# Performance work log

Measured on AMD Instinct MI355X. Metric: run time of the kernel, lower is better.

The kernel has to match this reference:

```python
import jax, jax.numpy as jnp
import numpy as np

B, S, F, H = 8, 4096, 1024, 1024


def setup_inputs() -> dict:
    key = jax.random.key(0)
    ks = jax.random.split(key, 7)
    sc = 1.0 / np.sqrt(F)
    return {
        "x": jax.random.normal(ks[0], (B, S, F), dtype=jnp.float32),
        "Wq": jax.random.normal(ks[1], (F, F), dtype=jnp.float32) * sc,
        "bq": jax.random.normal(ks[2], (F,), dtype=jnp.float32) * sc,
        "Wk": jax.random.normal(ks[3], (F, F), dtype=jnp.float32) * sc,
        "bk": jax.random.normal(ks[4], (F,), dtype=jnp.float32) * sc,
        "Wv": jax.random.normal(ks[5], (H, F), dtype=jnp.float32) * sc,
        "bv": jax.random.normal(ks[6], (H,), dtype=jnp.float32) * sc,
    }


def reference(x, Wq, bq, Wk, bk, Wv, bv):
    # q, k: [B, S, F]  (torch Linear: x @ W.T + b, W stored [out, in])
    q = jnp.einsum("bsf,of->bso", x, Wq) + bq
    k = jnp.einsum("bsf,of->bso", x, Wk) + bk
    # attention over the feature axis: logits [B, F, F], no scaling
    logits = jnp.einsum("bsf,bsg->bfg", q, k)
    weights = jax.nn.softmax(logits, axis=-1)
    # attn_out = x @ weights : [B, S, F]
    attn_out = jnp.einsum("bsf,bfg->bsg", x, weights)
    # value projection F -> H
    out = jnp.einsum("bsf,hf->bsh", attn_out, Wv) + bv
    return out
```

## Files before the change

kernel.cpp:

```cpp
#include <hip/hip_runtime.h>
#include <hip/hip_bf16.h>

#define DEVI __device__ __forceinline__

typedef _Float16 f16_t;
typedef f16_t f16x8 __attribute__((ext_vector_type(8)));
typedef f16_t f16x4 __attribute__((ext_vector_type(4)));
typedef float f32x4 __attribute__((ext_vector_type(4)));

static constexpr int B_ = 8, S_ = 4096, F_ = 1024, H_ = 1024;

DEVI void gload_lds16(const void* g, void* l) {
  __builtin_amdgcn_global_load_lds(
      (const __attribute__((address_space(1))) unsigned int*)g,
      (__attribute__((address_space(3))) unsigned int*)l, 16, 0, 0);
}

template <int MODE>
__global__ __launch_bounds__(256, 2) void gemm_nt(
    const f16_t* __restrict__ A0, const f16_t* __restrict__ A1,
    const f16_t* __restrict__ A2, const f16_t* __restrict__ B0,
    const f16_t* __restrict__ B1, const f16_t* __restrict__ B2,
    void* __restrict__ Cout, const float* __restrict__ bias,
    int Kseg, int nseg, int ldA, int ldB,
    long sA, long sB, long sC, int ldc, long noff)
{
  const int bz = blockIdx.z;
  const f16_t* Ab[3] = {A0 + (size_t)bz * sA, A1 + (size_t)bz * sA,
                        A2 + (size_t)bz * sA};
  const f16_t* Bb[3] = {B0 + (size_t)bz * sB, B1 + (size_t)bz * sB,
                        B2 + (size_t)bz * sB};
  const int tid = threadIdx.x;
  const int wave = tid >> 6, lane = tid & 63;
  const int wr = wave >> 1, wc = wave & 1;
  const long bm = (long)blockIdx.x * 128, bn = (long)blockIdx.y * 128;

  __shared__ f16_t As[128 * 64];
  __shared__ f16_t Bs[128 * 64];

  f32x4 acc[4][4] = {};

  const int l16 = lane * 16;
  const size_t lda_b = (size_t)ldA * 2;
  const size_t ldb_b = (size_t)ldB * 2;

  for (int seg = 0; seg < nseg; ++seg) {
    const char* Aseg = (const char*)Ab[seg];
    const char* Bseg = (const char*)Bb[seg];
    for (int kt = 0; kt < Kseg; kt += 64) {
      __syncthreads();
#pragma unroll
      for (int j = 0; j < 4; ++j) {
        const int base = j * 4096 + wave * 1024;
        const int off = base + l16;
        const int row = off >> 7, colb = off & 127;
        gload_lds16(Aseg + (size_t)(bm + row) * lda_b + (size_t)kt * 2 + colb,
                    (char*)As + base);
      }
#pragma unroll
      for (int j = 0; j < 4; ++j) {
        const int base = j * 4096 + wave * 1024;
        const int off = base + l16;
        const int row = off >> 7, colb = off & 127;
        gload_lds16(Bseg + (size_t)(bn + row) * ldb_b + (size_t)kt * 2 + colb,
                    (char*)Bs + base);
      }
      __syncthreads();
#pragma unroll
      for (int kk = 0; kk < 2; ++kk) {
        f16x8 af[4], bg[4];
#pragma unroll
        for (int m = 0; m < 4; ++m) {
          const int row = wr * 64 + m * 16 + (lane & 15);
          af[m] = *(const f16x8*)((const char*)As + row * 128 + kk * 64 + (lane >> 4) * 16);
        }
#pragma unroll
        for (int n = 0; n < 4; ++n) {
          const int row = wc * 64 + n * 16 + (lane & 15);
          bg[n] = *(const f16x8*)((const char*)Bs + row * 128 + kk * 64 + (lane >> 4) * 16);
        }
#pragma unroll
        for (int m = 0; m < 4; ++m)
#pragma unroll
          for (int n = 0; n < 4; ++n)
            acc[m][n] = __builtin_amdgcn_mfma_f32_16x16x32_f16(af[m], bg[n], acc[m][n], 0, 0, 0);
      }
    }
  }

  const int r0 = (lane >> 4) * 4;
  const int c0 = lane & 15;
#pragma unroll
  for (int m = 0; m < 4; ++m) {
#pragma unroll
    for (int n = 0; n < 4; ++n) {
      const long col = bn + wc * 64 + n * 16 + c0;
      float bcol = 0.f;
      if (MODE == 3) bcol = bias[col];
#pragma unroll
      for (int j = 0; j < 4; ++j) {
        const long row = bm + wr * 64 + m * 16 + r0 + j;
        const float vv = acc[m][n][j];
        if (MODE == 0 || MODE == 3) {
          ((float*)Cout)[(long)bz * sC + row * ldc + col] = vv + bcol;
        } else if (MODE == 1) {
          ((f16_t*)Cout)[(long)bz * sC + row * ldc + col] = (f16_t)vv;
        } else {
          f16_t hi = (f16_t)vv;
          float lo = vv - (float)hi;
          f16_t* C = (f16_t*)Cout + (long)bz * sC + row * ldc + col;
          C[0] = hi;
          C[noff] = (f16_t)lo;
        }
      }
    }
  }
}

__global__ __launch_bounds__(256) void conv_x(const float* __restrict__ x,
                                              f16_t* __restrict__ Xf,
                                              f16_t* __restrict__ Xt)
{
  const int b = blockIdx.z;
  const int s0 = blockIdx.x * 64, f0 = blockIdx.y * 64;
  const float* xb = x + (size_t)b * S_ * F_;
  f16_t* Xfb = Xf + (size_t)b * S_ * F_;
  f16_t* Xtb = Xt + (size_t)b * S_ * F_;
  __shared__ f16_t tile[64][72];
  const int tid = threadIdx.x;
#pragma unroll
  for (int i = 0; i < 4; ++i) {
    const int idx = i * 256 + tid;
    const int r = idx >> 4, c4 = idx & 15;
    f32x4 v = *(const f32x4*)(xb + (size_t)(s0 + r) * F_ + f0 + c4 * 4);
    f16x4 h;
    h[0] = (f16_t)v[0]; h[1] = (f16_t)v[1];
    h[2] = (f16_t)v[2]; h[3] = (f16_t)v[3];
    *(f16x4*)(Xfb + (size_t)(s0 + r) * F_ + f0 + c4 * 4) = h;
    *(f16x4*)(&tile[r][c4 * 4]) = h;
  }
  __syncthreads();
#pragma unroll
  for (int i = 0; i < 2; ++i) {
    const int idx = i * 256 + tid;
    const int r = idx >> 3, c8 = idx & 7;
    f16x8 o;
#pragma unroll
    for (int j = 0; j < 8; ++j) o[j] = tile[c8 * 8 + j][r];
    *(f16x8*)(Xtb + (size_t)(f0 + r) * S_ + s0 + c8 * 8) = o;
  }
}

__global__ __launch_bounds__(256) void conv_w(const float* __restrict__ Wq,
    const float* __restrict__ Wk, const float* __restrict__ Wv,
    f16_t* __restrict__ Wqh, f16_t* __restrict__ Wql,
    f16_t* __restrict__ Wkh, f16_t* __restrict__ Wkl,
    f16_t* __restrict__ Wvh)
{
  const int idx = blockIdx.x * 256 + threadIdx.x;
  const int e = idx * 4;
  f32x4 q = *(const f32x4*)(Wq + e);
  f32x4 k = *(const f32x4*)(Wk + e);
  f32x4 w = *(const f32x4*)(Wv + e);
  f16x4 qh, ql, kh, kl, wh;
#pragma unroll
  for (int j = 0; j < 4; ++j) {
    f16_t h = (f16_t)q[j];
    qh[j] = h; ql[j] = (f16_t)(q[j] - (float)h);
    h = (f16_t)k[j];
    kh[j] = h; kl[j] = (f16_t)(k[j] - (float)h);
    wh[j] = (f16_t)w[j];
  }
  *(f16x4*)(Wqh + e) = qh;
  *(f16x4*)(Wql + e) = ql;
  *(f16x4*)(Wkh + e) = kh;
  *(f16x4*)(Wkl + e) = kl;
  *(f16x4*)(Wvh + e) = wh;
}

__global__ __launch_bounds__(256) void colsum_k(const f16_t* __restrict__ Xt,
                                                float* __restrict__ c)
{
  const int gw = blockIdx.x * 4 + (threadIdx.x >> 6);
  const int lane = threadIdx.x & 63;
  const f16_t* row = Xt + (size_t)gw * S_;
  float s = 0.f;
#pragma unroll
  for (int rep = 0; rep < 8; ++rep) {
    f16x8 v = *(const f16x8*)(row + rep * 512 + lane * 8);
#pragma unroll
    for (int j = 0; j < 8; ++j) s += (float)v[j];
  }
#pragma unroll
  for (int off = 32; off > 0; off >>= 1) s += __shfl_down(s, off);
  if (lane == 0) c[gw] = s;
}

__global__ __launch_bounds__(256) void uv_k(const float* __restrict__ Wq,
    const float* __restrict__ Wk, const float* __restrict__ c,
    float* __restrict__ u, float* __restrict__ v)
{
  const int gw = blockIdx.x * 4 + (threadIdx.x >> 6);
  const int lane = threadIdx.x & 63;
  const int sel = gw >> 13;
  const int id = gw & 8191;
  const int b = id >> 10, f = id & 1023;
  const float* W = sel ? Wk : Wq;
  const float* wrow = W + (size_t)f * 1024;
  const float* crow = c + b * 1024;
  float s = 0.f;
#pragma unroll
  for (int rep = 0; rep < 4; ++rep) {
    f32x4 wv = *(const f32x4*)(wrow + rep * 256 + lane * 4);
    f32x4 cv = *(const f32x4*)(crow + rep * 256 + lane * 4);
    s += wv[0] * cv[0] + wv[1] * cv[1] + wv[2] * cv[2] + wv[3] * cv[3];
  }
#pragma unroll
  for (int off = 32; off > 0; off >>= 1) s += __shfl_down(s, off);
  if (lane == 0) { (sel ? v : u)[id] = s; }
}

__global__ __launch_bounds__(256) void softmax_k(const float* __restrict__ L,
    const float* __restrict__ bq, const float* __restrict__ bk,
    const float* __restrict__ u, const float* __restrict__ v,
    f16_t* __restrict__ W)
{
  const int row = blockIdx.x;
  const int b = row >> 10, f = row & 1023;
  const float* Lr = L + (size_t)row * 1024;
  const float uq = u[row], bqf = bq[f];
  const int tid = threadIdx.x;
  const int wave = tid >> 6, lane = tid & 63;

  f32x4 lv  = *(const f32x4*)(Lr + tid * 4);
  f32x4 bkv = *(const f32x4*)(bk + tid * 4);
  f32x4 vv  = *(const f32x4*)(v + b * 1024 + tid * 4);
  float lg[4];
#pragma unroll
  for (int j = 0; j < 4; ++j)
    lg[j] = lv[j] + uq * bkv[j] + bqf * (vv[j] + 4096.f * bkv[j]);

  __shared__ float red[8];
  float m = fmaxf(fmaxf(lg[0], lg[1]), fmaxf(lg[2], lg[3]));
#pragma unroll
  for (int off = 32; off > 0; off >>= 1) m = fmaxf(m, __shfl_down(m, off));
  if (lane == 0) red[wave] = m;
  __syncthreads();
  m = fmaxf(fmaxf(red[0], red[1]), fmaxf(red[2], red[3]));

  float p[4], s = 0.f;
#pragma unroll
  for (int j = 0; j < 4; ++j) { p[j] = __expf(lg[j] - m); s += p[j]; }
#pragma unroll
  for (int off = 32; off > 0; off >>= 1) s += __shfl_down(s, off);
  if (lane == 0) red[4 + wave] = s;
  __syncthreads();
  s = red[4] + red[5] + red[6] + red[7];
  const float inv = 1.f / s;
  f16x4 o;
#pragma unroll
  for (int j = 0; j < 4; ++j) o[j] = (f16_t)(p[j] * inv);
  *(f16x4*)(W + (size_t)row * 1024 + tid * 4) = o;
}

extern "C" void kernel_launch(void* const* d_in, const int* in_sizes, int n_in,
                              void* d_out, int out_size, void* d_ws, size_t ws_size,
                              hipStream_t stream)
{
  const float* x  = (const float*)d_in[0];
  const float* Wq = (const float*)d_in[1];
  const float* bq = (const float*)d_in[2];
  const float* Wk = (const float*)d_in[3];
  const float* bk = (const float*)d_in[4];
  const float* Wv = (const float*)d_in[5];
  const float* bv = (const float*)d_in[6];
  float* out = (float*)d_out;

  const size_t MB = 1024ull * 1024ull;
  char* ws = (char*)d_ws;
  f16_t* Xf  = (f16_t*)(ws);
  f16_t* Xt  = (f16_t*)(ws + 64 * MB);
  float* Lf  = (float*)(ws + 64 * MB);
  f16_t* Th  = (f16_t*)(ws + 96 * MB);
  f16_t* Tl  = (f16_t*)(ws + 112 * MB);
  f16_t* Wqh = (f16_t*)(ws + 128 * MB);
  f16_t* Wql = (f16_t*)(ws + 130 * MB);
  f16_t* Wkh = (f16_t*)(ws + 132 * MB);
  f16_t* Wkl = (f16_t*)(ws + 134 * MB);
  f16_t* Wvh = (f16_t*)(ws + 136 * MB);
  float* csum = (float*)(ws + 138 * MB);
  float* uvec = (float*)(ws + 138 * MB + 64 * 1024);
  float* vvec = (float*)(ws + 138 * MB + 128 * 1024);
  f16_t* Gh  = (f16_t*)(ws + 139 * MB);
  f16_t* Gl  = (f16_t*)(ws + 155 * MB);
  f16_t* Wsm = (f16_t*)(ws + 139 * MB);
  f16_t* Mt  = (f16_t*)(ws + 155 * MB);

  if (ws_size < 171 * MB) return;

  const long M1 = 1024L * 1024L;
  const long noffG = 8L * M1;
  const long noffT = 8L * M1;

  dim3 blk(256);
  conv_x<<<dim3(64, 16, 8), blk, 0, stream>>>(x, Xf, Xt);
  conv_w<<<dim3(1024), blk, 0, stream>>>(Wq, Wk, Wv, Wqh, Wql, Wkh, Wkl, Wvh);
  colsum_k<<<dim3(2048), blk, 0, stream>>>(Xt, csum);
  uv_k<<<dim3(4096), blk, 0, stream>>>(Wq, Wk, csum, uvec, vvec);
  gemm_nt<2><<<dim3(8, 8, 8), blk, 0, stream>>>(Xt, Xt, Xt, Xt, Xt, Xt,
      Gh, nullptr, 4096, 1, 4096, 4096,
      (long)F_ * S_, (long)F_ * S_, M1, 1024, noffG);
  gemm_nt<2><<<dim3(8, 8, 8), blk, 0, stream>>>(Wqh, Wql, Wqh, Gh, Gh, Gl,
      Th, nullptr, 1024, 3, 1024, 1024,
      0L, M1, M1, 1024, noffT);
  gemm_nt<0><<<dim3(8, 8, 8), blk, 0, stream>>>(Th, Tl, Th, Wkh, Wkh, Wkl,
      Lf, nullptr, 1024, 3, 1024, 1024,
      M1, 0L, M1, 1024, 0L);
  softmax_k<<<dim3(8192), blk, 0, stream>>>(Lf, bq, bk, uvec, vvec, Wsm);
  gemm_nt<1><<<dim3(8, 8, 8), blk, 0, stream>>>(Wvh, Wvh, Wvh, Wsm, Wsm, Wsm,
      Mt, nullptr, 1024, 1, 1024, 1024,
      0L, M1, M1, 1024, 0L);
  gemm_nt<3><<<dim3(32, 8, 8), blk, 0, stream>>>(Xf, Xf, Xf, Mt, Mt, Mt,
      out, bv, 1024, 1, 1024, 1024,
      (long)S_ * F_, M1, (long)S_ * H_, 1024, 0L);
}
```

Measured before the change: 641.3 us.

## Double-buffer LDS tiles and use 8-wave blocks in the GEMM kernel

The shared GEMM kernel now double-buffers its A and B LDS tiles and issues the next K-step's global-to-LDS loads before computing the current step. This aims to overlap memory latency with MFMA work and replaces two barriers per step with one. Blocks grow to 512 threads (8 waves in a 2x4 layout), so each wave owns a 64x32 sub-tile. The risks are doubled LDS use, which caps resident blocks, and tighter register limits from the new launch bounds, which could cause spills.

```diff
diff --git a/kernel.cpp b/kernel.cpp
--- a/kernel.cpp
+++ b/kernel.cpp
@@ -17,7 +17,7 @@
 }
 
 template <int MODE>
-__global__ __launch_bounds__(256, 2) void gemm_nt(
+__global__ __launch_bounds__(512, 4) void gemm_nt(
     const f16_t* __restrict__ A0, const f16_t* __restrict__ A1,
     const f16_t* __restrict__ A2, const f16_t* __restrict__ B0,
     const f16_t* __restrict__ B1, const f16_t* __restrict__ B2,
@@ -26,66 +26,72 @@
     long sA, long sB, long sC, int ldc, long noff)
 {
   const int bz = blockIdx.z;
-  const f16_t* Ab[3] = {A0 + (size_t)bz * sA, A1 + (size_t)bz * sA,
-                        A2 + (size_t)bz * sA};
-  const f16_t* Bb[3] = {B0 + (size_t)bz * sB, B1 + (size_t)bz * sB,
-                        B2 + (size_t)bz * sB};
   const int tid = threadIdx.x;
   const int wave = tid >> 6, lane = tid & 63;
-  const int wr = wave >> 1, wc = wave & 1;
+  const int wr = wave >> 2, wc = wave & 3;
   const long bm = (long)blockIdx.x * 128, bn = (long)blockIdx.y * 128;
 
-  __shared__ f16_t As[128 * 64];
-  __shared__ f16_t Bs[128 * 64];
-
-  f32x4 acc[4][4] = {};
-
-  const int l16 = lane * 16;
+  __shared__ f16_t As[2][128 * 64];
+  __shared__ f16_t Bs[2][128 * 64];
+
+  f32x4 acc[4][2] = {};
+
   const size_t lda_b = (size_t)ldA * 2;
   const size_t ldb_b = (size_t)ldB * 2;
 
-  for (int seg = 0; seg < nseg; ++seg) {
-    const char* Aseg = (const char*)Ab[seg];
-    const char* Bseg = (const char*)Bb[seg];
-    for (int kt = 0; kt < Kseg; kt += 64) {
-      __syncthreads();
-#pragma unroll
-      for (int j = 0; j < 4; ++j) {
-        const int base = j * 4096 + wave * 1024;
-        const int off = base + l16;
-        const int row = off >> 7, colb = off & 127;
-        gload_lds16(Aseg + (size_t)(bm + row) * lda_b + (size_t)kt * 2 + colb,
-                    (char*)As + base);
+  const char* A0b = (const char*)(A0 + (size_t)bz * sA);
+  const char* A1b = (const char*)(A1 + (size_t)bz * sA);
+  const char* A2b = (const char*)(A2 + (size_t)bz * sA);
+  const char* B0b = (const char*)(B0 + (size_t)bz * sB);
+  const char* B1b = (const char*)(B1 + (size_t)bz * sB);
+  const char* B2b = (const char*)(B2 + (size_t)bz * sB);
+
+  const int nsteps = nseg * (Kseg >> 6);
+
+  auto stage = [&](int buf, int sg, int kt) {
+    const char* Ap = (sg == 0) ? A0b : (sg == 1) ? A1b : A2b;
+    const char* Bp = (sg == 0) ? B0b : (sg == 1) ? B1b : B2b;
+    Ap += (size_t)kt * 2;
+    Bp += (size_t)kt * 2;
+#pragma unroll
+    for (int j = 0; j < 2; ++j) {
+      const int base = wave * 2048 + j * 1024;
+      const int off = base + lane * 16;
+      const int row = off >> 7, colb = off & 127;
+      gload_lds16(Ap + (size_t)(bm + row) * lda_b + colb, (char*)As[buf] + base);
+      gload_lds16(Bp + (size_t)(bn + row) * ldb_b + colb, (char*)Bs[buf] + base);
+    }
+  };
+
+  stage(0, 0, 0);
+  __syncthreads();
+
+  int seg = 0, kt = 0, cur = 0;
+  for (int t = 0; t < nsteps; ++t) {
+    int kt2 = kt + 64, seg2 = seg;
+    if (kt2 == Kseg) { kt2 = 0; seg2 = seg + 1; }
+    if (t + 1 < nsteps) stage(cur ^ 1, seg2, kt2);
+#pragma unroll
+    for (int kk = 0; kk < 2; ++kk) {
+      f16x8 af[4], bg[2];
+#pragma unroll
+      for (int m = 0; m < 4; ++m) {
+        const int row = wr * 64 + m * 16 + (lane & 15);
+        af[m] = *(const f16x8*)((const char*)As[cur] + row * 128 + kk * 64 + (lane >> 4) * 16);
       }
 #pragma unroll
-      for (int j = 0; j < 4; ++j) {
-        const int base = j * 4096 + wave * 1024;
-        const int off = base + l16;
-        const int row = off >> 7, colb = off & 127;
-        gload_lds16(Bseg + (size_t)(bn + row) * ldb_b + (size_t)kt * 2 + colb,
-                    (char*)Bs + base);
+      for (int n = 0; n < 2; ++n) {
+        const int row = wc * 32 + n * 16 + (lane & 15);
+        bg[n] = *(const f16x8*)((const char*)Bs[cur] + row * 128 + kk * 64 + (lane >> 4) * 16);
       }
-      __syncthreads();
-#pragma unroll
-      for (int kk = 0; kk < 2; ++kk) {
-        f16x8 af[4], bg[4];
-#pragma unroll
-        for (int m = 0; m < 4; ++m) {
-          const int row = wr * 64 + m * 16 + (lane & 15);
-          af[m] = *(const f16x8*)((const char*)As + row * 128 + kk * 64 + (lane >> 4) * 16);
-        }
-#pragma unroll
-        for (int n = 0; n < 4; ++n) {
-          const int row = wc * 64 + n * 16 + (lane & 15);
-          bg[n] = *(const f16x8*)((const char*)Bs + row * 128 + kk * 64 + (lane >> 4) * 16);
-        }
-#pragma unroll
-        for (int m = 0; m < 4; ++m)
-#pragma unroll
-          for (int n = 0; n < 4; ++n)
-            acc[m][n] = __builtin_amdgcn_mfma_f32_16x16x32_f16(af[m], bg[n], acc[m][n], 0, 0, 0);
-      }
+#pragma unroll
+      for (int m = 0; m < 4; ++m)
+#pragma unroll
+        for (int n = 0; n < 2; ++n)
+          acc[m][n] = __builtin_amdgcn_mfma_f32_16x16x32_f16(af[m], bg[n], acc[m][n], 0, 0, 0);
     }
+    __syncthreads();
+    cur ^= 1; seg = seg2; kt = kt2;
   }
 
   const int r0 = (lane >> 4) * 4;
@@ -93,8 +99,8 @@
 #pragma unroll
   for (int m = 0; m < 4; ++m) {
 #pragma unroll
-    for (int n = 0; n < 4; ++n) {
-      const long col = bn + wc * 64 + n * 16 + c0;
+    for (int n = 0; n < 2; ++n) {
+      const long col = bn + wc * 32 + n * 16 + c0;
       float bcol = 0.f;
       if (MODE == 3) bcol = bias[col];
 #pragma unroll
@@ -303,24 +309,25 @@
   const long noffT = 8L * M1;
 
   dim3 blk(256);
+  dim3 gblk(512);
   conv_x<<<dim3(64, 16, 8), blk, 0, stream>>>(x, Xf, Xt);
   conv_w<<<dim3(1024), blk, 0, stream>>>(Wq, Wk, Wv, Wqh, Wql, Wkh, Wkl, Wvh);
   colsum_k<<<dim3(2048), blk, 0, stream>>>(Xt, csum);
   uv_k<<<dim3(4096), blk, 0, stream>>>(Wq, Wk, csum, uvec, vvec);
-  gemm_nt<2><<<dim3(8, 8, 8), blk, 0, stream>>>(Xt, Xt, Xt, Xt, Xt, Xt,
+  gemm_nt<2><<<dim3(8, 8, 8), gblk, 0, stream>>>(Xt, Xt, Xt, Xt, Xt, Xt,
       Gh, nullptr, 4096, 1, 4096, 4096,
       (long)F_ * S_, (long)F_ * S_, M1, 1024, noffG);
-  gemm_nt<2><<<dim3(8, 8, 8), blk, 0, stream>>>(Wqh, Wql, Wqh, Gh, Gh, Gl,
+  gemm_nt<2><<<dim3(8, 8, 8), gblk, 0, stream>>>(Wqh, Wql, Wqh, Gh, Gh, Gl,
       Th, nullptr, 1024, 3, 1024, 1024,
       0L, M1, M1, 1024, noffT);
-  gemm_nt<0><<<dim3(8, 8, 8), blk, 0, stream>>>(Th, Tl, Th, Wkh, Wkh, Wkl,
+  gemm_nt<0><<<dim3(8, 8, 8), gblk, 0, stream>>>(Th, Tl, Th, Wkh, Wkh, Wkl,
       Lf, nullptr, 1024, 3, 1024, 1024,
       M1, 0L, M1, 1024, 0L);
   softmax_k<<<dim3(8192), blk, 0, stream>>>(Lf, bq, bk, uvec, vvec, Wsm);
-  gemm_nt<1><<<dim3(8, 8, 8), blk, 0, stream>>>(Wvh, Wvh, Wvh, Wsm, Wsm, Wsm,
+  gemm_nt<1><<<dim3(8, 8, 8), gblk, 0, stream>>>(Wvh, Wvh, Wvh, Wsm, Wsm, Wsm,
       Mt, nullptr, 1024, 1, 1024, 1024,
       0L, M1, M1, 1024, 0L);
-  gemm_nt<3><<<dim3(32, 8, 8), blk, 0, stream>>>(Xf, Xf, Xf, Mt, Mt, Mt,
+  gemm_nt<3><<<dim3(32, 8, 8), gblk, 0, stream>>>(Xf, Xf, Xf, Mt, Mt, Mt,
       out, bv, 1024, 1, 1024, 1024,
       (long)S_ * F_, M1, (long)S_ * H_, 1024, 0L);
 }
```

After: 1.387 ms. +116.3%, slower.
